# Kernel optimization log

Hardware: AMD Instinct MI355X
Metric: run time of the kernel (lower is better)

## Reference

```python
import jax, jax.numpy as jnp
import numpy as np

GRID_SIZE = 10
DEGREE = 3


def bspline_basis(x, grid_size=GRID_SIZE, degree=DEGREE):
    """Cox-de Boor B-spline basis on a uniform grid over [-1, 1].
    x: (...,) -> (..., grid_size + degree)
    """
    h = 2.0 / grid_size
    # extended knot vector, length grid_size + 2*degree + 1
    knots = jnp.arange(-degree, grid_size + degree + 1, dtype=x.dtype) * h - 1.0
    # keep inputs inside the grid support (standard KAN practice)
    x = jnp.clip(x, -1.0, 1.0 - 1e-6)
    xe = x[..., None]
    b = ((xe >= knots[:-1]) & (xe < knots[1:])).astype(x.dtype)  # degree-0, (..., K-1)
    for d in range(1, degree + 1):
        left = (xe - knots[: -(d + 1)]) / (knots[d:-1] - knots[: -(d + 1)]) * b[..., :-1]
        right = (knots[d + 1:] - xe) / (knots[d + 1:] - knots[1:-d]) * b[..., 1:]
        b = left + right
    return b  # (..., grid_size + degree)


def setup_inputs() -> dict:
    key = jax.random.key(0)
    k1, k2, k3 = jax.random.split(key, 3)
    B, S, IN, OUT, E = 4, 2048, 256, 256, 8
    n_basis = GRID_SIZE + DEGREE
    x = jax.random.normal(k1, (B, S, IN), dtype=jnp.float32)
    coeff = jax.random.normal(k2, (E, n_basis), dtype=jnp.float32) * 0.1
    gating_weights = jax.random.normal(k3, (IN, OUT, E), dtype=jnp.float32)
    return {"x": x, "coeff": coeff, "gating_weights": gating_weights}


def reference(x, coeff, gating_weights):
    # spline experts: elementwise basis eval, then per-expert linear combo
    basis = bspline_basis(x)                              # (B, S, I, n_basis)
    expert_outputs = jnp.einsum('bsin,en->bsie', basis, coeff)  # (B, S, I, E)
    gates = jax.nn.softmax(gating_weights, axis=-1)       # (I, O, E)
    out = jnp.einsum('bsie,ioe->bso', expert_outputs, gates)
    return out
```

## Files before the change

### kernel.cpp

```cpp
#include <hip/hip_runtime.h>

typedef __attribute__((ext_vector_type(8))) short short8;
typedef __attribute__((ext_vector_type(4))) float f32x4;

#define IN_DIM 256
#define OUT_DIM 256
#define NB 16
#define KDIM (IN_DIM * NB)
#define TM 32
#define TN 128
#define BK 128
#define STEPS (IN_DIM / 8)
#define ABUF (TM * BK * 2)
#define BBUF (TN * BK * 2)

__device__ __forceinline__ unsigned short f2bf(float f) {
  union { float f; unsigned int u; } v; v.f = f;
  unsigned int r = v.u + 0x7fffu + ((v.u >> 16) & 1u);
  return (unsigned short)(r >> 16);
}

__device__ __forceinline__ void glds16(const void* g, void* l) {
  __builtin_amdgcn_global_load_lds((__attribute__((address_space(1))) const void*)g,
                                   (__attribute__((address_space(3))) void*)l, 16, 0, 0);
}

__device__ __forceinline__ void spline_row(float xv, unsigned* d) {
  float xc = fminf(fmaxf(xv, -1.0f), 1.0f - 1e-6f);
  float u = (xc + 1.0f) * 5.0f;
  int c = (int)u;
  c = c > 9 ? 9 : (c < 0 ? 0 : c);
  float tt = u - (float)c;
  float omt = 1.0f - tt;
  float t2 = tt * tt, t3 = t2 * tt;
  float b0 = omt * omt * omt * (1.0f / 6.0f);
  float b1 = (3.0f * t3 - 6.0f * t2 + 4.0f) * (1.0f / 6.0f);
  float b2 = (-3.0f * t3 + 3.0f * t2 + 3.0f * tt + 1.0f) * (1.0f / 6.0f);
  float b3 = t3 * (1.0f / 6.0f);
  unsigned h0 = f2bf(b0), h1 = f2bf(b1), h2 = f2bf(b2), h3 = f2bf(b3);
  const int a = c >> 1;
  const bool odd = (c & 1) != 0;
  unsigned p01 = h0 | (h1 << 16);
  unsigned p23 = h2 | (h3 << 16);
  unsigned A0 = odd ? (h0 << 16) : p01;
  unsigned A1 = odd ? (h1 | (h2 << 16)) : p23;
  unsigned A2 = odd ? h3 : 0u;
#pragma unroll
  for (int j = 0; j < 8; ++j) {
    unsigned v = (j == a) ? A0 : 0u;
    v = (j == a + 1) ? A1 : v;
    v = (j == a + 2) ? A2 : v;
    d[j] = v;
  }
}

__global__ __launch_bounds__(256) void kan_prep(const float* __restrict__ coeff,
                                                const float* __restrict__ gw,
                                                unsigned short* __restrict__ BmT) {
  __shared__ float csh[104];
  __shared__ unsigned short tile[16][256];
  const int t = threadIdx.x;
  if (t < 104) csh[t] = coeff[t];
  __syncthreads();
  const int otile = blockIdx.x, itile = blockIdx.y;
  const int il = t >> 4, ol = t & 15;
  const int i = itile * 16 + il;
  const int o = otile * 16 + ol;
  const float* g = gw + (size_t)(i * OUT_DIM + o) * 8;
  float4 g0 = *(const float4*)g;
  float4 g1 = *(const float4*)(g + 4);
  float ge[8] = {g0.x, g0.y, g0.z, g0.w, g1.x, g1.y, g1.z, g1.w};
  float mx = ge[0];
#pragma unroll
  for (int e = 1; e < 8; ++e) mx = fmaxf(mx, ge[e]);
  float p[8]; float s = 0.f;
#pragma unroll
  for (int e = 0; e < 8; ++e) { p[e] = __expf(ge[e] - mx); s += p[e]; }
  const float inv = 1.0f / s;
  unsigned short row[16];
#pragma unroll
  for (int n = 0; n < 13; ++n) {
    float w = 0.f;
#pragma unroll
    for (int e = 0; e < 8; ++e) w += p[e] * csh[e * 13 + n];
    row[n] = f2bf(w * inv);
  }
  row[13] = 0; row[14] = 0; row[15] = 0;
  int4* dst = (int4*)&tile[ol][il * 16];
  dst[0] = *(const int4*)&row[0];
  dst[1] = *(const int4*)&row[8];
  __syncthreads();
  const int oo = t >> 4, ck = t & 15;
  int4 v0 = *(const int4*)&tile[oo][ck * 16];
  int4 v1 = *(const int4*)&tile[oo][ck * 16 + 8];
  int4* out4 = (int4*)(BmT + (size_t)(otile * 16 + oo) * KDIM + itile * 256 + ck * 16);
  out4[0] = v0;
  out4[1] = v1;
}

__global__ __launch_bounds__(256, 2) void kan_gemm(const float* __restrict__ x,
                                                   const unsigned short* __restrict__ BmT,
                                                   float* __restrict__ out) {
  __shared__ unsigned short Ash[2][TM * BK];
  __shared__ unsigned short Bsh[2][TN * BK];

  const int t = threadIdx.x;
  const int lane = t & 63;
  const int wave = t >> 6;
  const int wn = wave;
  const int mb = blockIdx.x * TM;
  const int ob = blockIdx.y * TN;

  const int r = t & 31;
  const int il = t >> 5;
  const float* xptr = x + (size_t)(mb + r) * IN_DIM + il;
  char* const abase = (char*)&Ash[0][0] + r * 256;
  const int msw = r & 7;
  const int aw0 = ((2 * il + 0) ^ msw) << 4;
  const int aw1 = ((2 * il + 1) ^ msw) << 4;

  const unsigned short* bgbase =
      BmT + (size_t)(ob + (t >> 4)) * KDIM + ((t & 15) ^ ((t >> 4) & 7)) * 8;
  char* const bl = (char*)&Bsh[0][0] + wave * 1024;

  f32x4 acc[2][2];
#pragma unroll
  for (int a = 0; a < 2; ++a)
#pragma unroll
    for (int b = 0; b < 2; ++b) acc[a][b] = (f32x4){0.f, 0.f, 0.f, 0.f};

  int aoff[2], boff[2];
#pragma unroll
  for (int f = 0; f < 2; ++f) {
    const int ro = f * 16 + (lane & 15);
    aoff[f] = ro * 256 + (((lane >> 4) ^ (ro & 7)) << 4);
    const int bo = wn * 32 + f * 16 + (lane & 15);
    boff[f] = bo * 256 + (((lane >> 4) ^ (bo & 7)) << 4);
  }

  {
#pragma unroll
    for (int q = 0; q < 8; ++q)
      glds16(bgbase + (size_t)q * 16 * KDIM, bl + q * 4096);
    float xv = *xptr;
    unsigned d[8];
    spline_row(xv, d);
    *(int4*)(abase + aw0) = *(const int4*)&d[0];
    *(int4*)(abase + aw1) = *(const int4*)&d[4];
    asm volatile("s_waitcnt vmcnt(0)" ::: "memory");
  }

  for (int s = 0; s < STEPS; ++s) {
    __syncthreads();
    const int cur = s & 1;
    float xn = 0.f;
    if (s + 1 < STEPS) {
      xn = xptr[(s + 1) * 8];
#pragma unroll
      for (int q = 0; q < 8; ++q)
        glds16(bgbase + (size_t)(s + 1) * BK + (size_t)q * 16 * KDIM,
               bl + (1 - cur) * BBUF + q * 4096);
    }
    const char* Ac = (const char*)&Ash[0][0] + cur * ABUF;
    const char* Bc = (const char*)&Bsh[0][0] + cur * BBUF;
    __builtin_amdgcn_s_setprio(1);
#pragma unroll
    for (int kc = 0; kc < 4; ++kc) {
      short8 af[2], bfr[2];
#pragma unroll
      for (int f = 0; f < 2; ++f) af[f] = *(const short8*)(Ac + (aoff[f] ^ (kc << 6)));
#pragma unroll
      for (int f = 0; f < 2; ++f) bfr[f] = *(const short8*)(Bc + (boff[f] ^ (kc << 6)));
#pragma unroll
      for (int mf = 0; mf < 2; ++mf)
#pragma unroll
        for (int nf = 0; nf < 2; ++nf)
          acc[mf][nf] = __builtin_amdgcn_mfma_f32_16x16x32_bf16(af[mf], bfr[nf], acc[mf][nf], 0, 0, 0);
    }
    __builtin_amdgcn_s_setprio(0);
    if (s + 1 < STEPS) {
      unsigned d[8];
      spline_row(xn, d);
      char* an = abase + (1 - cur) * ABUF;
      *(int4*)(an + aw0) = *(const int4*)&d[0];
      *(int4*)(an + aw1) = *(const int4*)&d[4];
    }
  }

#pragma unroll
  for (int mf = 0; mf < 2; ++mf)
#pragma unroll
    for (int nf = 0; nf < 2; ++nf)
#pragma unroll
      for (int q = 0; q < 4; ++q) {
        int row = mb + mf * 16 + ((lane >> 4) << 2) + q;
        int col = ob + wn * 32 + nf * 16 + (lane & 15);
        out[(size_t)row * OUT_DIM + col] = acc[mf][nf][q];
      }
}

extern "C" void kernel_launch(void* const* d_in, const int* in_sizes, int n_in,
                              void* d_out, int out_size, void* d_ws, size_t ws_size,
                              hipStream_t stream) {
  const float* x     = (const float*)d_in[0];
  const float* coeff = (const float*)d_in[1];
  const float* gw    = (const float*)d_in[2];
  float* out = (float*)d_out;
  unsigned short* BmT = (unsigned short*)d_ws;

  kan_prep<<<dim3(16, 16), dim3(256), 0, stream>>>(coeff, gw, BmT);
  dim3 grid(8192 / TM, OUT_DIM / TN);
  kan_gemm<<<grid, dim3(256), 0, stream>>>(x, BmT, out);
}
```

Measured before the change: 105.1 us.

## Load gate-weight B fragments directly from global and retile to 64x64

Removes the LDS staging of the precomputed B matrix. Each wave now reads its bf16 B fragments straight from global memory (L2-resident) into registers, while only the spline-basis A tile stays in LDS. The block tile changes from 32x128 to 64x64 with a 2x2 wave layout, and each thread computes two spline rows per step. This cuts LDS traffic and the async-copy waits, but relies on global-load latency being hidden without prefetch, and raises total B reads because there are more blocks.

```diff
diff --git a/kernel.cpp b/kernel.cpp
--- a/kernel.cpp
+++ b/kernel.cpp
@@ -7,22 +7,16 @@
 #define OUT_DIM 256
 #define NB 16
 #define KDIM (IN_DIM * NB)
-#define TM 32
-#define TN 128
+#define TM 64
+#define TN 64
 #define BK 128
-#define STEPS (IN_DIM / 8)
-#define ABUF (TM * BK * 2)
-#define BBUF (TN * BK * 2)
+#define STEPS 32
+#define ABUF 16384
 
 __device__ __forceinline__ unsigned short f2bf(float f) {
   union { float f; unsigned int u; } v; v.f = f;
   unsigned int r = v.u + 0x7fffu + ((v.u >> 16) & 1u);
   return (unsigned short)(r >> 16);
-}
-
-__device__ __forceinline__ void glds16(const void* g, void* l) {
-  __builtin_amdgcn_global_load_lds((__attribute__((address_space(1))) const void*)g,
-                                   (__attribute__((address_space(3))) void*)l, 16, 0, 0);
 }
 
 __device__ __forceinline__ void spline_row(float xv, unsigned* d) {
@@ -102,26 +96,38 @@
                                                    const unsigned short* __restrict__ BmT,
                                                    float* __restrict__ out) {
   __shared__ unsigned short Ash[2][TM * BK];
-  __shared__ unsigned short Bsh[2][TN * BK];
 
   const int t = threadIdx.x;
   const int lane = t & 63;
   const int wave = t >> 6;
-  const int wn = wave;
+  const int wm = wave >> 1, wn = wave & 1;
   const int mb = blockIdx.x * TM;
   const int ob = blockIdx.y * TN;
 
-  const int r = t & 31;
-  const int il = t >> 5;
-  const float* xptr = x + (size_t)(mb + r) * IN_DIM + il;
-  char* const abase = (char*)&Ash[0][0] + r * 256;
+  const int r = t >> 2, ip = t & 3;
+  const float* xp = x + (size_t)(mb + r) * IN_DIM + 2 * ip;
+  char* const ab0 = (char*)&Ash[0][0] + r * 256;
   const int msw = r & 7;
-  const int aw0 = ((2 * il + 0) ^ msw) << 4;
-  const int aw1 = ((2 * il + 1) ^ msw) << 4;
-
-  const unsigned short* bgbase =
-      BmT + (size_t)(ob + (t >> 4)) * KDIM + ((t & 15) ^ ((t >> 4) & 7)) * 8;
-  char* const bl = (char*)&Bsh[0][0] + wave * 1024;
+  const int aw0 = ((4 * ip + 0) ^ msw) << 4;
+  const int aw1 = ((4 * ip + 1) ^ msw) << 4;
+  const int aw2 = ((4 * ip + 2) ^ msw) << 4;
+  const int aw3 = ((4 * ip + 3) ^ msw) << 4;
+
+  const int rl = lane & 15, qd = lane >> 4;
+
+  const unsigned short* bp[2];
+#pragma unroll
+  for (int f = 0; f < 2; ++f)
+    bp[f] = BmT + (size_t)(ob + wn * 32 + f * 16 + rl) * KDIM + qd * 8;
+
+  int aadr[4][2];
+#pragma unroll
+  for (int ks = 0; ks < 4; ++ks)
+#pragma unroll
+    for (int f = 0; f < 2; ++f) {
+      const int ro = wm * 32 + f * 16 + rl;
+      aadr[ks][f] = ro * 256 + (((qd | (ks << 2)) ^ (ro & 7)) << 4);
+    }
 
   f32x4 acc[2][2];
 #pragma unroll
@@ -129,62 +135,51 @@
 #pragma unroll
     for (int b = 0; b < 2; ++b) acc[a][b] = (f32x4){0.f, 0.f, 0.f, 0.f};
 
-  int aoff[2], boff[2];
-#pragma unroll
-  for (int f = 0; f < 2; ++f) {
-    const int ro = f * 16 + (lane & 15);
-    aoff[f] = ro * 256 + (((lane >> 4) ^ (ro & 7)) << 4);
-    const int bo = wn * 32 + f * 16 + (lane & 15);
-    boff[f] = bo * 256 + (((lane >> 4) ^ (bo & 7)) << 4);
-  }
-
   {
-#pragma unroll
-    for (int q = 0; q < 8; ++q)
-      glds16(bgbase + (size_t)q * 16 * KDIM, bl + q * 4096);
-    float xv = *xptr;
+    float2 xv = *(const float2*)xp;
     unsigned d[8];
-    spline_row(xv, d);
-    *(int4*)(abase + aw0) = *(const int4*)&d[0];
-    *(int4*)(abase + aw1) = *(const int4*)&d[4];
-    asm volatile("s_waitcnt vmcnt(0)" ::: "memory");
+    spline_row(xv.x, d);
+    *(int4*)(ab0 + aw0) = *(const int4*)&d[0];
+    *(int4*)(ab0 + aw1) = *(const int4*)&d[4];
+    spline_row(xv.y, d);
+    *(int4*)(ab0 + aw2) = *(const int4*)&d[0];
+    *(int4*)(ab0 + aw3) = *(const int4*)&d[4];
+    asm volatile("s_waitcnt lgkmcnt(0)" ::: "memory");
+    __builtin_amdgcn_sched_barrier(0);
+    __builtin_amdgcn_s_barrier();
   }
 
   for (int s = 0; s < STEPS; ++s) {
-    __syncthreads();
     const int cur = s & 1;
-    float xn = 0.f;
-    if (s + 1 < STEPS) {
-      xn = xptr[(s + 1) * 8];
-#pragma unroll
-      for (int q = 0; q < 8; ++q)
-        glds16(bgbase + (size_t)(s + 1) * BK + (size_t)q * 16 * KDIM,
-               bl + (1 - cur) * BBUF + q * 4096);
-    }
+    float2 xn = {0.f, 0.f};
+    if (s + 1 < STEPS) xn = *(const float2*)(xp + 8 * (s + 1));
     const char* Ac = (const char*)&Ash[0][0] + cur * ABUF;
-    const char* Bc = (const char*)&Bsh[0][0] + cur * BBUF;
-    __builtin_amdgcn_s_setprio(1);
-#pragma unroll
-    for (int kc = 0; kc < 4; ++kc) {
-      short8 af[2], bfr[2];
-#pragma unroll
-      for (int f = 0; f < 2; ++f) af[f] = *(const short8*)(Ac + (aoff[f] ^ (kc << 6)));
-#pragma unroll
-      for (int f = 0; f < 2; ++f) bfr[f] = *(const short8*)(Bc + (boff[f] ^ (kc << 6)));
+#pragma unroll
+    for (int ks = 0; ks < 4; ++ks) {
+      short8 bfr[2], af[2];
+#pragma unroll
+      for (int f = 0; f < 2; ++f) bfr[f] = *(const short8*)(bp[f] + s * 128 + ks * 32);
+#pragma unroll
+      for (int f = 0; f < 2; ++f) af[f] = *(const short8*)(Ac + aadr[ks][f]);
 #pragma unroll
       for (int mf = 0; mf < 2; ++mf)
 #pragma unroll
         for (int nf = 0; nf < 2; ++nf)
           acc[mf][nf] = __builtin_amdgcn_mfma_f32_16x16x32_bf16(af[mf], bfr[nf], acc[mf][nf], 0, 0, 0);
     }
-    __builtin_amdgcn_s_setprio(0);
     if (s + 1 < STEPS) {
       unsigned d[8];
-      spline_row(xn, d);
-      char* an = abase + (1 - cur) * ABUF;
+      char* an = ab0 + (1 - cur) * ABUF;
+      spline_row(xn.x, d);
       *(int4*)(an + aw0) = *(const int4*)&d[0];
       *(int4*)(an + aw1) = *(const int4*)&d[4];
+      spline_row(xn.y, d);
+      *(int4*)(an + aw2) = *(const int4*)&d[0];
+      *(int4*)(an + aw3) = *(const int4*)&d[4];
     }
+    asm volatile("s_waitcnt lgkmcnt(0)" ::: "memory");
+    __builtin_amdgcn_sched_barrier(0);
+    __builtin_amdgcn_s_barrier();
   }
 
 #pragma unroll
@@ -193,8 +188,8 @@
     for (int nf = 0; nf < 2; ++nf)
 #pragma unroll
       for (int q = 0; q < 4; ++q) {
-        int row = mb + mf * 16 + ((lane >> 4) << 2) + q;
-        int col = ob + wn * 32 + nf * 16 + (lane & 15);
+        int row = mb + wm * 32 + mf * 16 + (qd << 2) + q;
+        int col = ob + wn * 32 + nf * 16 + rl;
         out[(size_t)row * OUT_DIM + col] = acc[mf][nf][q];
       }
 }
```

Measured after the change: 131.0 us. 24.6% more time.
